# Performance work log

Measured on AMD Instinct MI355X. Metric: run time of the kernel, lower is better.

The kernel has to match this reference:

```python
import jax, jax.numpy as jnp
import numpy as np

N, E, IN_F, H1, F1, H2, F2, OUT_F = 50000, 800000, 128, 4, 32, 1, 64, 2
NEG_SLOPE = 0.2  # PyG GATConv default


def setup_inputs() -> dict:
    key = jax.random.key(0)
    ks = jax.random.split(key, 10)
    p = lambda k, shp: jax.random.normal(k, shp, jnp.float32) * 0.1
    return {
        "x": jax.random.normal(ks[0], (N, IN_F), jnp.float32),
        "edge_index": jax.random.randint(ks[1], (2, E), 0, N),
        "W1": p(ks[2], (IN_F, H1 * F1)),
        "att_s1": p(ks[3], (H1, F1)),
        "att_d1": p(ks[4], (H1, F1)),
        "b1": jnp.zeros((H1 * F1,), jnp.float32),
        "W2": p(ks[5], (H1 * F1, H2 * F2)),
        "att_s2": p(ks[6], (H2, F2)),
        "att_d2": p(ks[7], (H2, F2)),
        "b2": jnp.zeros((F2,), jnp.float32),
        "Wl": p(ks[8], (F2, OUT_F)),
        "bl": jnp.zeros((OUT_F,), jnp.float32),
    }


def _gat_conv(x, src, dst, W, att_s, att_d, bias, concat):
    # PyG GATConv: per-head linear, leaky-relu attention logits,
    # segment-softmax over incoming edges of each dst, scatter-add aggregate.
    n = x.shape[0]
    H, F = att_s.shape
    h = (x @ W).reshape(n, H, F)                        # [N, H, F]
    a_s = jnp.einsum('nhf,hf->nh', h, att_s)            # [N, H]
    a_d = jnp.einsum('nhf,hf->nh', h, att_d)
    logits = jax.nn.leaky_relu(a_s[src] + a_d[dst], NEG_SLOPE)  # [Etot, H]
    m = jax.ops.segment_max(logits, dst, num_segments=n)
    e = jnp.exp(logits - m[dst])
    denom = jax.ops.segment_sum(e, dst, num_segments=n)
    alpha = e / denom[dst]                              # segment softmax
    msg = h[src] * alpha[:, :, None]                    # [Etot, H, F]
    out = jax.ops.segment_sum(msg, dst, num_segments=n)  # [N, H, F]
    out = out.reshape(n, H * F) if concat else out.mean(axis=1)
    return out + bias


def reference(x, edge_index, W1, att_s1, att_d1, b1, W2, att_s2, att_d2, b2, Wl, bl):
    n = x.shape[0]
    loops = jnp.arange(n, dtype=edge_index.dtype)       # add_self_loops=True
    src = jnp.concatenate([edge_index[0], loops])
    dst = jnp.concatenate([edge_index[1], loops])
    h = jax.nn.elu(_gat_conv(x, src, dst, W1, att_s1, att_d1, b1, True))
    h = jax.nn.elu(_gat_conv(h, src, dst, W2, att_s2, att_d2, b2, False))
    pooled = h.sum(axis=0, keepdims=True)               # global_add_pool, batch=0
    out = pooled @ Wl + bl
    return pooled, out
```

## Files before the change

kernel.cpp:

```cpp
#include <hip/hip_runtime.h>

#define N_NODES 50000
#define N_EDGES 800000
#define NB 196
#define P1_BLOCKS 256
#define EPB 3125
#define BH_SIZE (NB * P1_BLOCKS)
#define GEMM_BLOCKS ((N_NODES + 63) / 64)
#define AGG_BLOCKS (N_NODES / 4)

__device__ __forceinline__ float lrelu(float x) { return fmaxf(x, 0.2f * x); }
__device__ __forceinline__ float elu(float x) { return x > 0.f ? x : __expf(x) - 1.f; }

typedef float f32x2 __attribute__((ext_vector_type(2)));
typedef float f32x4v __attribute__((ext_vector_type(4)));
typedef short bf16x8 __attribute__((ext_vector_type(8)));

__device__ __forceinline__ unsigned f2bf_rn(float x) {
  unsigned u = __float_as_uint(x);
  return (u + 0x7fffu + ((u >> 16) & 1u)) >> 16;
}
__device__ __forceinline__ unsigned pack2bf(float a, float b) {
  return f2bf_rn(a) | (f2bf_rn(b) << 16);
}
__device__ __forceinline__ uint4 pack8bf(const float* v) {
  uint4 o;
  o.x = pack2bf(v[0], v[1]); o.y = pack2bf(v[2], v[3]);
  o.z = pack2bf(v[4], v[5]); o.w = pack2bf(v[6], v[7]);
  return o;
}

__device__ __forceinline__ int block_excl_scan(int v, int* total_out) {
  int lane = threadIdx.x & 63;
  int wid = threadIdx.x >> 6;
  int x = v;
#pragma unroll
  for (int off = 1; off < 64; off <<= 1) {
    int u = __shfl_up(x, off);
    if (lane >= off) x += u;
  }
  __shared__ int wsum[4];
  if (lane == 63) wsum[wid] = x;
  __syncthreads();
  int add = 0;
#pragma unroll
  for (int k = 0; k < 4; ++k)
    if (k < wid) add += wsum[k];
  if (total_out) *total_out = wsum[0] + wsum[1] + wsum[2] + wsum[3];
  return x + add - v;
}

__global__ __launch_bounds__(256) void setup_hist_kernel(
    const int* __restrict__ ei, int* __restrict__ bh,
    const float* __restrict__ W1, const float* __restrict__ atts1, const float* __restrict__ attd1,
    const float* __restrict__ W2, const float* __restrict__ atts2, const float* __restrict__ attd2,
    uint4* __restrict__ Wpk1, uint4* __restrict__ Wpk2) {
  __shared__ int cnt[NB];
  int bid = blockIdx.x;
  if (bid >= 2) {
    for (int t = threadIdx.x; t < NB; t += 256) cnt[t] = 0;
    __syncthreads();
    int start = (bid - 2) * EPB;
    for (int i = start + threadIdx.x; i < start + EPB; i += 256)
      atomicAdd(&cnt[ei[N_EDGES + i] >> 8], 1);
    __syncthreads();
    for (int t = threadIdx.x; t < NB; t += 256)
      bh[t * P1_BLOCKS + (bid - 2)] = cnt[t];
    return;
  }
  if (bid == 0) {
    for (int s = threadIdx.x; s < 4 * 9 * 64; s += 256) {
      int l = s & 63, sf = s >> 6;
      int f = sf % 9, ks = sf / 9;
      int colb = f * 16 + (l & 15);
      int kb = ks * 32 + ((l >> 4) << 3);
      float v[8];
      if (colb < 128) {
#pragma unroll
        for (int j = 0; j < 8; ++j) v[j] = W1[(kb + j) * 128 + colb];
      } else if (colb < 136) {
        int cc = colb - 128;
        const float* at = (cc < 4) ? atts1 : attd1;
        int h = cc & 3;
#pragma unroll
        for (int j = 0; j < 8; ++j) {
          float s2 = 0.f;
          for (int q = 0; q < 32; ++q) s2 += W1[(kb + j) * 128 + h * 32 + q] * at[h * 32 + q];
          v[j] = s2;
        }
      } else {
#pragma unroll
        for (int j = 0; j < 8; ++j) v[j] = 0.f;
      }
      Wpk1[s] = pack8bf(v);
    }
  } else {
    for (int s = threadIdx.x; s < 4 * 5 * 64; s += 256) {
      int l = s & 63, sf = s >> 6;
      int f = sf % 5, ks = sf / 5;
      int colb = f * 16 + (l & 15);
      int kb = ks * 32 + ((l >> 4) << 3);
      float v[8];
      if (colb < 64) {
#pragma unroll
        for (int j = 0; j < 8; ++j) v[j] = W2[(kb + j) * 64 + colb];
      } else if (colb < 66) {
        const float* at = (colb == 64) ? atts2 : attd2;
#pragma unroll
        for (int j = 0; j < 8; ++j) {
          float s2 = 0.f;
          for (int q = 0; q < 64; ++q) s2 += W2[(kb + j) * 64 + q] * at[q];
          v[j] = s2;
        }
      } else {
#pragma unroll
        for (int j = 0; j < 8; ++j) v[j] = 0.f;
      }
      Wpk2[s] = pack8bf(v);
    }
  }
}

template <int NF, bool ABF16>
__device__ __forceinline__ void mfma_gemm_body(int bx, const void* __restrict__ Ap,
                                               const uint4* __restrict__ Wpk,
                                               unsigned* __restrict__ Yb,
                                               float* __restrict__ as_out, float* __restrict__ ad_out) {
  __shared__ unsigned short Xs[64 * 136];
  __shared__ uint4 Ws[NF * 256];
  int t = threadIdx.x;
  int rbase = bx * 64;
#pragma unroll
  for (int p = 0; p < NF; ++p) Ws[p * 256 + t] = Wpk[p * 256 + t];
  if constexpr (ABF16) {
    const uint4* A4 = (const uint4*)Ap;
#pragma unroll
    for (int p = 0; p < 4; ++p) {
      int i = p * 256 + t;
      int row = i >> 4, q = i & 15;
      int gr = rbase + row; if (gr > N_NODES - 1) gr = N_NODES - 1;
      *(uint4*)&Xs[row * 136 + q * 8] = A4[gr * 16 + q];
    }
  } else {
    const float4* A4 = (const float4*)Ap;
#pragma unroll
    for (int p = 0; p < 8; ++p) {
      int i = p * 256 + t;
      int row = i >> 5, q = i & 31;
      int gr = rbase + row; if (gr > N_NODES - 1) gr = N_NODES - 1;
      float4 v = A4[gr * 32 + q];
      *(uint2*)&Xs[row * 136 + q * 4] = make_uint2(pack2bf(v.x, v.y), pack2bf(v.z, v.w));
    }
  }
  __syncthreads();

  int l = t & 63, wv = t >> 6;
  int lc = l & 15, lk = l >> 4;
  f32x4v acc[NF];
#pragma unroll
  for (int f = 0; f < NF; ++f) acc[f] = (f32x4v){0.f, 0.f, 0.f, 0.f};
  const unsigned short* ap = &Xs[(wv * 16 + lc) * 136 + lk * 8];
#pragma unroll
  for (int ks = 0; ks < 4; ++ks) {
    bf16x8 a = *(const bf16x8*)(ap + ks * 32);
#pragma unroll
    for (int f = 0; f < NF; ++f) {
      bf16x8 b = *(const bf16x8*)&Ws[(ks * NF + f) * 64 + l];
      acc[f] = __builtin_amdgcn_mfma_f32_16x16x32_bf16(a, b, acc[f], 0, 0, 0);
    }
  }

  constexpr int NCF = NF - 1;
#pragma unroll
  for (int reg = 0; reg < 4; ++reg) {
    int row = rbase + wv * 16 + lk * 4 + reg;
    bool rok = row < N_NODES;
    float av = acc[NCF][reg];
    if (rok) {
      if constexpr (NF == 9) {
        if (lc < 4) as_out[row * 4 + lc] = av;
        else if (lc < 8) ad_out[row * 4 + lc - 4] = av;
      } else {
        if (lc == 0) as_out[row] = av;
        else if (lc == 1) ad_out[row] = av;
      }
    }
    unsigned words[NCF];
#pragma unroll
    for (int f = 0; f < NCF; ++f) {
      float v = acc[f][reg];
      float n1 = __shfl_xor(v, 1);
      unsigned pk = (unsigned)__builtin_amdgcn_cvt_pk_fp8_f32(v, n1, 0, false);
      unsigned pk2 = (unsigned)__shfl_xor((int)pk, 2);
      words[f] = (pk & 0xffffu) | (pk2 << 16);
    }
    if (rok && (lc & 3) == 0) {
#pragma unroll
      for (int f = 0; f < NCF; ++f)
        Yb[row * (NCF * 4) + f * 4 + (lc >> 2)] = words[f];
    }
  }
}

__global__ __launch_bounds__(256) void gemm128_scan_kernel(
    const float* __restrict__ x, const uint4* __restrict__ Wpk1,
    unsigned* __restrict__ h1b, float* __restrict__ as1, float* __restrict__ ad1,
    const int* __restrict__ bh, int* __restrict__ bhP, int* __restrict__ blocksum) {
  if (blockIdx.x < GEMM_BLOCKS) {
    mfma_gemm_body<9, false>(blockIdx.x, x, Wpk1, h1b, as1, ad1);
  } else {
    int b = blockIdx.x - GEMM_BLOCKS;
    int g = b * 256 + threadIdx.x;
    int v = bh[g];
    int total;
    int ex = block_excl_scan(v, &total);
    bhP[g] = ex;
    if (threadIdx.x == 0) blocksum[b] = total;
  }
}

__global__ __launch_bounds__(256) void gemm64_kernel(const uint4* __restrict__ h1eb,
                                                     const uint4* __restrict__ Wpk2,
                                                     unsigned* __restrict__ h2b,
                                                     float* __restrict__ as2, float* __restrict__ ad2) {
  mfma_gemm_body<5, true>(blockIdx.x, h1eb, Wpk2, h2b, as2, ad2);
}

__global__ __launch_bounds__(256) void scatter1_kernel(const int* __restrict__ ei, const int* __restrict__ bhP,
                                                       const int* __restrict__ blocksum, int2* __restrict__ eb) {
  __shared__ int cur[NB];
  __shared__ int boff[NB];
  int t = threadIdx.x;
  for (int i = t; i < NB; i += 256) cur[i] = 0;
  {
    int v = (t < NB) ? blocksum[t] : 0;
    int ex = block_excl_scan(v, nullptr);
    if (t < NB) boff[t] = ex;
  }
  __syncthreads();
  int start = blockIdx.x * EPB;
  for (int i = start + t; i < start + EPB; i += 256) {
    int dst = ei[N_EDGES + i];
    int src = ei[i];
    int bin = dst >> 8;
    int r = atomicAdd(&cur[bin], 1);
    int idx = bin * P1_BLOCKS + blockIdx.x;
    int pos = bhP[idx] + boff[bin] + r;
    eb[pos] = make_int2(src, dst);
  }
}

__global__ __launch_bounds__(256) void bucket_csr_kernel(const int2* __restrict__ eb,
                                                         const int* __restrict__ blocksum,
                                                         int* __restrict__ rowptrF, int* __restrict__ col) {
  __shared__ int cnt[256];
  __shared__ int basel[256];
  __shared__ int cur[256];
  __shared__ int sse[2];
  int b = blockIdx.x;
  int t = threadIdx.x;
  {
    int v = (t < NB) ? blocksum[t] : 0;
    int ex0 = block_excl_scan(v, nullptr);
    if (t == b) sse[0] = ex0;
    if (t == b + 1) sse[1] = ex0;
  }
  cnt[t] = 0;
  cur[t] = 0;
  __syncthreads();
  int start = sse[0];
  int end = (b == NB - 1) ? N_EDGES : sse[1];
  for (int i = start + t; i < end; i += 256)
    atomicAdd(&cnt[eb[i].y & 255], 1);
  __syncthreads();
  int ex = block_excl_scan(cnt[t], nullptr);
  basel[t] = start + ex;
  int g = b * 256 + t;
  if (g < N_NODES) rowptrF[g] = start + ex;
  if (g == N_NODES) rowptrF[N_NODES] = N_EDGES;
  __syncthreads();
  for (int i = start + t; i < end; i += 256) {
    int2 e = eb[i];
    int d8 = e.y & 255;
    int r = atomicAdd(&cur[d8], 1);
    col[basel[d8] + r] = e.x;
  }
}

__global__ __launch_bounds__(256) void agg1_kernel(const uint2* __restrict__ h1f8, const int* __restrict__ rowptr,
                                                   const int* __restrict__ col, const float* __restrict__ as1,
                                                   const float* __restrict__ ad1, const float4* __restrict__ b1v,
                                                   uint4* __restrict__ h1eb4) {
  int n = (blockIdx.x * 256 + threadIdx.x) >> 6;
  int lane = threadIdx.x & 63;
  int slot = lane >> 4;
  int fo = lane & 15;
  int h = fo >> 2;
  int beg = rowptr[n], end = rowptr[n + 1];
  float adh = ad1[n * 4 + h];

  f32x2 acc2[4];
#pragma unroll
  for (int j = 0; j < 4; ++j) acc2[j] = (f32x2){0.f, 0.f};
  float esum = 0.f;

#define ACC_EDGE1(E)                                               \
  {                                                                \
    int src = col[E];                                              \
    float a = __expf(lrelu(as1[src * 4 + h] + adh));               \
    esum += a;                                                     \
    f32x2 av = {a, a};                                             \
    uint2 uu = h1f8[src * 16 + fo];                                \
    f32x2 p0 = __builtin_amdgcn_cvt_pk_f32_fp8(uu.x, false);       \
    f32x2 p1 = __builtin_amdgcn_cvt_pk_f32_fp8(uu.x, true);        \
    f32x2 p2 = __builtin_amdgcn_cvt_pk_f32_fp8(uu.y, false);       \
    f32x2 p3 = __builtin_amdgcn_cvt_pk_f32_fp8(uu.y, true);        \
    acc2[0] += av * p0; acc2[1] += av * p1;                        \
    acc2[2] += av * p2; acc2[3] += av * p3;                        \
  }

  int i = beg;
  for (; i + 16 <= end; i += 16) {
#pragma unroll
    for (int u = 0; u < 4; ++u) ACC_EDGE1(i + u * 4 + slot);
  }
  for (; i + 4 <= end; i += 4) ACC_EDGE1(i + slot);
  int rem = end - i;
  if (slot < rem) ACC_EDGE1(i + slot);
#undef ACC_EDGE1
  if (slot == 0) {
    float a = __expf(lrelu(as1[n * 4 + h] + adh));
    esum += a;
    f32x2 av = {a, a};
    uint2 uu = h1f8[n * 16 + fo];
    f32x2 p0 = __builtin_amdgcn_cvt_pk_f32_fp8(uu.x, false);
    f32x2 p1 = __builtin_amdgcn_cvt_pk_f32_fp8(uu.x, true);
    f32x2 p2 = __builtin_amdgcn_cvt_pk_f32_fp8(uu.y, false);
    f32x2 p3 = __builtin_amdgcn_cvt_pk_f32_fp8(uu.y, true);
    acc2[0] += av * p0; acc2[1] += av * p1;
    acc2[2] += av * p2; acc2[3] += av * p3;
  }
#pragma unroll
  for (int j = 0; j < 4; ++j) {
    acc2[j].x += __shfl_xor(acc2[j].x, 16);
    acc2[j].y += __shfl_xor(acc2[j].y, 16);
    acc2[j].x += __shfl_xor(acc2[j].x, 32);
    acc2[j].y += __shfl_xor(acc2[j].y, 32);
  }
  esum += __shfl_xor(esum, 16);
  esum += __shfl_xor(esum, 32);
  if (slot == 0) {
    float dsc = 1.f / esum;
    float4 b0 = b1v[fo * 2], b1 = b1v[fo * 2 + 1];
    float f0 = elu(acc2[0].x * dsc + b0.x), f1 = elu(acc2[0].y * dsc + b0.y);
    float f2 = elu(acc2[1].x * dsc + b0.z), f3 = elu(acc2[1].y * dsc + b0.w);
    float f4 = elu(acc2[2].x * dsc + b1.x), f5 = elu(acc2[2].y * dsc + b1.y);
    float f6 = elu(acc2[3].x * dsc + b1.z), f7 = elu(acc2[3].y * dsc + b1.w);
    uint4 o;
    o.x = pack2bf(f0, f1); o.y = pack2bf(f2, f3);
    o.z = pack2bf(f4, f5); o.w = pack2bf(f6, f7);
    h1eb4[n * 16 + fo] = o;
  }
}

__global__ __launch_bounds__(256) void agg2_kernel(const uint2* __restrict__ h2f8, const int* __restrict__ rowptr,
                                                   const int* __restrict__ col, const float* __restrict__ as2,
                                                   const float* __restrict__ ad2, const float4* __restrict__ b2v,
                                                   float* __restrict__ pooled) {
  __shared__ float red[4][64];
  int n = (blockIdx.x * 256 + threadIdx.x) >> 6;
  int lane = threadIdx.x & 63;
  int wid = threadIdx.x >> 6;
  int slot = lane >> 3;
  int fo = lane & 7;
  int beg = rowptr[n], end = rowptr[n + 1];
  float ad = ad2[n];

  f32x2 acc2[4];
#pragma unroll
  for (int j = 0; j < 4; ++j) acc2[j] = (f32x2){0.f, 0.f};
  float esum = 0.f;

#define ACC_EDGE2(E)                                               \
  {                                                                \
    int src = col[E];                                              \
    float a = __expf(lrelu(as2[src] + ad));                        \
    esum += a;                                                     \
    f32x2 av = {a, a};                                             \
    uint2 uu = h2f8[src * 8 + fo];                                 \
    f32x2 p0 = __builtin_amdgcn_cvt_pk_f32_fp8(uu.x, false);       \
    f32x2 p1 = __builtin_amdgcn_cvt_pk_f32_fp8(uu.x, true);        \
    f32x2 p2 = __builtin_amdgcn_cvt_pk_f32_fp8(uu.y, false);       \
    f32x2 p3 = __builtin_amdgcn_cvt_pk_f32_fp8(uu.y, true);        \
    acc2[0] += av * p0; acc2[1] += av * p1;                        \
    acc2[2] += av * p2; acc2[3] += av * p3;                        \
  }

  int i = beg;
  for (; i + 32 <= end; i += 32) {
#pragma unroll
    for (int u = 0; u < 4; ++u) ACC_EDGE2(i + u * 8 + slot);
  }
  for (; i + 8 <= end; i += 8) ACC_EDGE2(i + slot);
  int rem = end - i;
  if (slot < rem) ACC_EDGE2(i + slot);
#undef ACC_EDGE2
  if (slot == 0) {
    float a = __expf(lrelu(as2[n] + ad));
    esum += a;
    f32x2 av = {a, a};
    uint2 uu = h2f8[n * 8 + fo];
    f32x2 p0 = __builtin_amdgcn_cvt_pk_f32_fp8(uu.x, false);
    f32x2 p1 = __builtin_amdgcn_cvt_pk_f32_fp8(uu.x, true);
    f32x2 p2 = __builtin_amdgcn_cvt_pk_f32_fp8(uu.y, false);
    f32x2 p3 = __builtin_amdgcn_cvt_pk_f32_fp8(uu.y, true);
    acc2[0] += av * p0; acc2[1] += av * p1;
    acc2[2] += av * p2; acc2[3] += av * p3;
  }
#pragma unroll
  for (int j = 0; j < 4; ++j) {
#pragma unroll
    for (int off = 8; off <= 32; off <<= 1) {
      acc2[j].x += __shfl_xor(acc2[j].x, off);
      acc2[j].y += __shfl_xor(acc2[j].y, off);
    }
  }
  esum += __shfl_xor(esum, 8);
  esum += __shfl_xor(esum, 16);
  esum += __shfl_xor(esum, 32);
  if (slot == 0) {
    float dsc = 1.f / esum;
    float4 b0 = b2v[fo * 2], b1 = b2v[fo * 2 + 1];
    red[wid][fo * 8 + 0] = elu(acc2[0].x * dsc + b0.x);
    red[wid][fo * 8 + 1] = elu(acc2[0].y * dsc + b0.y);
    red[wid][fo * 8 + 2] = elu(acc2[1].x * dsc + b0.z);
    red[wid][fo * 8 + 3] = elu(acc2[1].y * dsc + b0.w);
    red[wid][fo * 8 + 4] = elu(acc2[2].x * dsc + b1.x);
    red[wid][fo * 8 + 5] = elu(acc2[2].y * dsc + b1.y);
    red[wid][fo * 8 + 6] = elu(acc2[3].x * dsc + b1.z);
    red[wid][fo * 8 + 7] = elu(acc2[3].y * dsc + b1.w);
  }
  __syncthreads();
  if (threadIdx.x < 64) {
    float sum = red[0][threadIdx.x] + red[1][threadIdx.x] + red[2][threadIdx.x] + red[3][threadIdx.x];
    atomicAdd(&pooled[(blockIdx.x & 63) * 64 + threadIdx.x], sum);
  }
}

__global__ void final_kernel(const float* __restrict__ pooledS, const float* __restrict__ Wl,
                             const float* __restrict__ bl, float* __restrict__ out) {
  __shared__ float p[64];
  int t = threadIdx.x;
  float v = 0.f;
  for (int k = 0; k < 64; ++k) v += pooledS[k * 64 + t];
  p[t] = v;
  out[t] = v;
  __syncthreads();
  if (t < 2) {
    float s = bl[t];
    for (int k = 0; k < 64; ++k) s += p[k] * Wl[k * 2 + t];
    out[64 + t] = s;
  }
}

extern "C" void kernel_launch(void* const* d_in, const int* in_sizes, int n_in,
                              void* d_out, int out_size, void* d_ws, size_t ws_size,
                              hipStream_t stream) {
  (void)in_sizes; (void)n_in; (void)out_size; (void)ws_size;
  const float* x     = (const float*)d_in[0];
  const int*   ei    = (const int*)d_in[1];
  const float* W1    = (const float*)d_in[2];
  const float* atts1 = (const float*)d_in[3];
  const float* attd1 = (const float*)d_in[4];
  const float* b1    = (const float*)d_in[5];
  const float* W2    = (const float*)d_in[6];
  const float* atts2 = (const float*)d_in[7];
  const float* attd2 = (const float*)d_in[8];
  const float* b2    = (const float*)d_in[9];
  const float* Wl    = (const float*)d_in[10];
  const float* bl    = (const float*)d_in[11];
  float* out = (float*)d_out;

  char* w = (char*)d_ws;
  unsigned* h1b  = (unsigned*)w; w += (size_t)N_NODES * 128;
  unsigned* h1eb = (unsigned*)w; w += (size_t)N_NODES * 128 * 2;
  unsigned* h2b  = (unsigned*)w; w += (size_t)N_NODES * 64;
  float* as1  = (float*)w; w += (size_t)N_NODES * 16;
  float* ad1  = (float*)w; w += (size_t)N_NODES * 16;
  float* as2  = (float*)w; w += (size_t)N_NODES * 4;
  float* ad2  = (float*)w; w += (size_t)N_NODES * 4;
  float* pooled = (float*)w; w += 64 * 64 * 4;
  uint4* Wpk1 = (uint4*)w; w += 4 * 9 * 64 * 16;
  uint4* Wpk2 = (uint4*)w; w += 4 * 5 * 64 * 16;
  int* rowptrF = (int*)w; w += (size_t)(N_NODES + 1) * 4 + 12;
  int* col    = (int*)w; w += (size_t)N_EDGES * 4;
  int2* eb    = (int2*)w; w += (size_t)N_EDGES * 8;
  int* bh     = (int*)w; w += (size_t)BH_SIZE * 4;
  int* bhP    = (int*)w; w += (size_t)BH_SIZE * 4;
  int* blocksum = (int*)w; w += 256 * 4;

  (void)hipMemsetAsync(pooled, 0, 64 * 64 * 4, stream);

  setup_hist_kernel<<<258, 256, 0, stream>>>(ei, bh, W1, atts1, attd1, W2, atts2, attd2, Wpk1, Wpk2);
  gemm128_scan_kernel<<<GEMM_BLOCKS + NB, 256, 0, stream>>>(x, Wpk1, h1b, as1, ad1, bh, bhP, blocksum);
  scatter1_kernel<<<P1_BLOCKS, 256, 0, stream>>>(ei, bhP, blocksum, eb);
  bucket_csr_kernel<<<NB, 256, 0, stream>>>(eb, blocksum, rowptrF, col);
  agg1_kernel<<<AGG_BLOCKS, 256, 0, stream>>>((const uint2*)h1b, rowptrF, col, as1, ad1,
                                              (const float4*)b1, (uint4*)h1eb);
  gemm64_kernel<<<GEMM_BLOCKS, 256, 0, stream>>>((const uint4*)h1eb, Wpk2, h2b, as2, ad2);
  agg2_kernel<<<AGG_BLOCKS, 256, 0, stream>>>((const uint2*)h2b, rowptrF, col, as2, ad2,
                                              (const float4*)b2, pooled);
  final_kernel<<<1, 64, 0, stream>>>(pooled, Wl, bl, out);
}
```

Measured before the change: 206.1 us.

## Pack bucketed edges to 32-bit, stage buckets in LDS, shrink GEMM weight smem

Scatter now writes each bucketed edge as one 32-bit word (16-bit src plus the low 8 bits of dst) instead of an int2, halving that intermediate buffer's traffic. bucket_csr caches its bucket in shared memory when it fits, so the second pass reads LDS instead of global memory. The GEMM body loads weights one k-slice at a time into a smaller shared buffer, which adds barriers per k-step but cuts LDS use and may raise occupancy. The pooled memset is folded into the setup kernel, saving one launch. The 16-bit src packing only works because N is below 65536.

```diff
diff --git a/kernel.cpp b/kernel.cpp
--- a/kernel.cpp
+++ b/kernel.cpp
@@ -8,6 +8,7 @@
 #define BH_SIZE (NB * P1_BLOCKS)
 #define GEMM_BLOCKS ((N_NODES + 63) / 64)
 #define AGG_BLOCKS (N_NODES / 4)
+#define EBS_CAP 5120
 
 __device__ __forceinline__ float lrelu(float x) { return fmaxf(x, 0.2f * x); }
 __device__ __forceinline__ float elu(float x) { return x > 0.f ? x : __expf(x) - 1.f; }
@@ -54,7 +55,7 @@
     const int* __restrict__ ei, int* __restrict__ bh,
     const float* __restrict__ W1, const float* __restrict__ atts1, const float* __restrict__ attd1,
     const float* __restrict__ W2, const float* __restrict__ atts2, const float* __restrict__ attd2,
-    uint4* __restrict__ Wpk1, uint4* __restrict__ Wpk2) {
+    uint4* __restrict__ Wpk1, uint4* __restrict__ Wpk2, float* __restrict__ pooled) {
   __shared__ int cnt[NB];
   int bid = blockIdx.x;
   if (bid >= 2) {
@@ -118,6 +119,7 @@
       }
       Wpk2[s] = pack8bf(v);
     }
+    for (int i = threadIdx.x; i < 64 * 64; i += 256) pooled[i] = 0.f;
   }
 }
 
@@ -127,11 +129,9 @@
                                                unsigned* __restrict__ Yb,
                                                float* __restrict__ as_out, float* __restrict__ ad_out) {
   __shared__ unsigned short Xs[64 * 136];
-  __shared__ uint4 Ws[NF * 256];
+  __shared__ uint4 Ws[NF * 64];
   int t = threadIdx.x;
   int rbase = bx * 64;
-#pragma unroll
-  for (int p = 0; p < NF; ++p) Ws[p * 256 + t] = Wpk[p * 256 + t];
   if constexpr (ABF16) {
     const uint4* A4 = (const uint4*)Ap;
 #pragma unroll
@@ -152,7 +152,6 @@
       *(uint2*)&Xs[row * 136 + q * 4] = make_uint2(pack2bf(v.x, v.y), pack2bf(v.z, v.w));
     }
   }
-  __syncthreads();
 
   int l = t & 63, wv = t >> 6;
   int lc = l & 15, lk = l >> 4;
@@ -162,12 +161,15 @@
   const unsigned short* ap = &Xs[(wv * 16 + lc) * 136 + lk * 8];
 #pragma unroll
   for (int ks = 0; ks < 4; ++ks) {
+    for (int i = t; i < NF * 64; i += 256) Ws[i] = Wpk[ks * NF * 64 + i];
+    __syncthreads();
     bf16x8 a = *(const bf16x8*)(ap + ks * 32);
 #pragma unroll
     for (int f = 0; f < NF; ++f) {
-      bf16x8 b = *(const bf16x8*)&Ws[(ks * NF + f) * 64 + l];
+      bf16x8 b = *(const bf16x8*)&Ws[f * 64 + l];
       acc[f] = __builtin_amdgcn_mfma_f32_16x16x32_bf16(a, b, acc[f], 0, 0, 0);
     }
+    if (ks < 3) __syncthreads();
   }
 
   constexpr int NCF = NF - 1;
@@ -227,7 +229,7 @@
 }
 
 __global__ __launch_bounds__(256) void scatter1_kernel(const int* __restrict__ ei, const int* __restrict__ bhP,
-                                                       const int* __restrict__ blocksum, int2* __restrict__ eb) {
+                                                       const int* __restrict__ blocksum, unsigned* __restrict__ eb) {
   __shared__ int cur[NB];
   __shared__ int boff[NB];
   int t = threadIdx.x;
@@ -246,13 +248,14 @@
     int r = atomicAdd(&cur[bin], 1);
     int idx = bin * P1_BLOCKS + blockIdx.x;
     int pos = bhP[idx] + boff[bin] + r;
-    eb[pos] = make_int2(src, dst);
-  }
-}
-
-__global__ __launch_bounds__(256) void bucket_csr_kernel(const int2* __restrict__ eb,
+    eb[pos] = (unsigned)src | ((unsigned)(dst & 255) << 16);
+  }
+}
+
+__global__ __launch_bounds__(256) void bucket_csr_kernel(const unsigned* __restrict__ eb,
                                                          const int* __restrict__ blocksum,
                                                          int* __restrict__ rowptrF, int* __restrict__ col) {
+  __shared__ unsigned ebs[EBS_CAP];
   __shared__ int cnt[256];
   __shared__ int basel[256];
   __shared__ int cur[256];
@@ -270,8 +273,13 @@
   __syncthreads();
   int start = sse[0];
   int end = (b == NB - 1) ? N_EDGES : sse[1];
-  for (int i = start + t; i < end; i += 256)
-    atomicAdd(&cnt[eb[i].y & 255], 1);
+  int m = end - start;
+  bool fits = (m <= EBS_CAP);
+  for (int i = t; i < m; i += 256) {
+    unsigned e = eb[start + i];
+    if (fits) ebs[i] = e;
+    atomicAdd(&cnt[e >> 16], 1);
+  }
   __syncthreads();
   int ex = block_excl_scan(cnt[t], nullptr);
   basel[t] = start + ex;
@@ -279,11 +287,11 @@
   if (g < N_NODES) rowptrF[g] = start + ex;
   if (g == N_NODES) rowptrF[N_NODES] = N_EDGES;
   __syncthreads();
-  for (int i = start + t; i < end; i += 256) {
-    int2 e = eb[i];
-    int d8 = e.y & 255;
+  for (int i = t; i < m; i += 256) {
+    unsigned e = fits ? ebs[i] : eb[start + i];
+    int d8 = e >> 16;
     int r = atomicAdd(&cur[d8], 1);
-    col[basel[d8] + r] = e.x;
+    col[basel[d8] + r] = (int)(e & 0xffffu);
   }
 }
 
@@ -314,7 +322,7 @@
     f32x2 p0 = __builtin_amdgcn_cvt_pk_f32_fp8(uu.x, false);       \
     f32x2 p1 = __builtin_amdgcn_cvt_pk_f32_fp8(uu.x, true);        \
     f32x2 p2 = __builtin_amdgcn_cvt_pk_f32_fp8(uu.y, false);       \
-    f32x2 p3 = __builtin_amdgcn_cvt_pk_f32_fp8(uu.y, true);        \
+    f32x2 p3 = __builtin_amdgcn_cvt_pk_f32_fp8(uu.y, true);       \
     acc2[0] += av * p0; acc2[1] += av * p1;                        \
     acc2[2] += av * p2; acc2[3] += av * p3;                        \
   }
@@ -391,7 +399,7 @@
     f32x2 p0 = __builtin_amdgcn_cvt_pk_f32_fp8(uu.x, false);       \
     f32x2 p1 = __builtin_amdgcn_cvt_pk_f32_fp8(uu.x, true);        \
     f32x2 p2 = __builtin_amdgcn_cvt_pk_f32_fp8(uu.y, false);       \
-    f32x2 p3 = __builtin_amdgcn_cvt_pk_f32_fp8(uu.y, true);        \
+    f32x2 p3 = __builtin_amdgcn_cvt_pk_f32_fp8(uu.y, true);       \
     acc2[0] += av * p0; acc2[1] += av * p1;                        \
     acc2[2] += av * p2; acc2[3] += av * p3;                        \
   }
@@ -494,14 +502,13 @@
   uint4* Wpk2 = (uint4*)w; w += 4 * 5 * 64 * 16;
   int* rowptrF = (int*)w; w += (size_t)(N_NODES + 1) * 4 + 12;
   int* col    = (int*)w; w += (size_t)N_EDGES * 4;
-  int2* eb    = (int2*)w; w += (size_t)N_EDGES * 8;
+  unsigned* eb = (unsigned*)w; w += (size_t)N_EDGES * 4;
   int* bh     = (int*)w; w += (size_t)BH_SIZE * 4;
   int* bhP    = (int*)w; w += (size_t)BH_SIZE * 4;
   int* blocksum = (int*)w; w += 256 * 4;
 
-  (void)hipMemsetAsync(pooled, 0, 64 * 64 * 4, stream);
-
-  setup_hist_kernel<<<258, 256, 0, stream>>>(ei, bh, W1, atts1, attd1, W2, atts2, attd2, Wpk1, Wpk2);
+  setup_hist_kernel<<<258, 256, 0, stream>>>(ei, bh, W1, atts1, attd1, W2, atts2, attd2,
+                                             Wpk1, Wpk2, pooled);
   gemm128_scan_kernel<<<GEMM_BLOCKS + NB, 256, 0, stream>>>(x, Wpk1, h1b, as1, ad1, bh, bhP, blocksum);
   scatter1_kernel<<<P1_BLOCKS, 256, 0, stream>>>(ei, bhP, blocksum, eb);
   bucket_csr_kernel<<<NB, 256, 0, stream>>>(eb, blocksum, rowptrF, col);
```

Result: no change. 204.9 us (-0.6%).
